# Kernel optimization log

Measured on AMD Instinct MI355X. Metric: run time of the kernel, lower is better.

Reference implementation:

```python
import jax, jax.numpy as jnp
import numpy as np

EPS = float(np.finfo(float).eps)
NUM_RFS = 1

def conv3d(x, w):
    # x: [N,C,D,H,W], w: [O,I,kd,kh,kw], VALID, stride 1 (matches F.conv3d defaults)
    return jax.lax.conv_general_dilated(
        x, w, window_strides=(1, 1, 1), padding='VALID',
        dimension_numbers=('NCDHW', 'OIDHW', 'NCDHW'))

def setup_inputs() -> dict:
    key = jax.random.key(0)
    k1, k2, k3, k4 = jax.random.split(key, 4)
    x = jax.random.normal(k1, (1, 1, 3, 394, 394), jnp.float32)
    x_prev = jax.random.normal(k2, (1, 1, 3, 394, 394), jnp.float32)
    # params stored post-permute as [out_ch, in_ch, kt, kh, kw]
    filts_temp = jax.random.normal(k3, (16, 1, 3, 11, 11), jnp.float32)
    filts_notemp = jax.random.normal(k4, (16, 1, 1, 11, 11), jnp.float32)
    return {"x": x, "x_prev": x_prev, "filts_temp": filts_temp, "filts_notemp": filts_notemp}

def reference(x, x_prev, filts_temp, filts_notemp):
    corr_x = NUM_RFS * filts_temp.shape[3]  # kh
    corr_y = NUM_RFS * filts_temp.shape[4]  # kw
    num_filts = filts_temp.shape[0] + filts_notemp.shape[0]

    def feats(v):
        vt = jax.nn.relu(conv3d(v, filts_temp)) / 2           # [1,16,1,H',W'] (T==kt)
        vn = jax.nn.relu(conv3d(v[:, :, -1:, :, :], filts_notemp))  # last frame, [1,16,1,H',W']
        return jnp.concatenate([vt, vn], axis=1)              # [1,32,1,H',W']

    f = feats(x)
    fp = feats(x_prev)
    # channel-wise normalization
    x1 = f / (jnp.sum(f, axis=1, keepdims=True) + EPS)
    x1_prev = fp / (jnp.sum(fp, axis=1, keepdims=True) + EPS)

    y_max, x_max = x1.shape[3], x1.shape[4]
    yc = y_max - 2 * corr_y
    xc = x_max - 2 * corr_x
    # cropped current-frame channels become conv filters: [nf,1,1,yc,xc]
    x1_filts = x1[:, :, :, corr_y:y_max - corr_y, corr_x:x_max - corr_x].reshape(
        num_filts, 1, 1, yc, xc)
    prev = x1_prev.reshape(1, 1, num_filts, y_max, x_max)
    # normalized cross-correlation via conv3d: out [1, nf, nf, 2cy+1, 2cx+1]
    x2 = conv3d(prev, x1_filts)
    x2 = x2.reshape(1, num_filts, num_filts, 2 * corr_y + 1, 2 * corr_x + 1)
    x2 = x2 / ((y_max - 2 * corr_y) * (x_max - 2 * corr_y))  # faithful to original (uses corr_y twice)
    return x1, x2
```

## Files before the change

### kernel.cpp

```cpp
#include <hip/hip_runtime.h>
#include <hip/hip_bf16.h>


typedef unsigned short ushort_t;
typedef unsigned int uint_t;
typedef unsigned char uchar_t;
typedef __attribute__((ext_vector_type(4))) float f32x4;
typedef __attribute__((ext_vector_type(16))) float f32x16;
typedef __attribute__((ext_vector_type(4))) uint_t uint4_t;
typedef __attribute__((ext_vector_type(2))) uint_t uint2_t;
typedef __attribute__((ext_vector_type(8))) int int8v;

#define EPSF 2.2204460492503131e-16f
#define X1_N (32*384*384)
#define X2_N (32*32*23*23)

#define FILTB_ROW_B 12288
#define FILTB_BYTES (372*48*32*8)
#define PREVB_STRIDE 432
#define PREVB_BYTES (32*385*PREVB_STRIDE)
#define ZERO_BYTES ((size_t)FILTB_BYTES + PREVB_BYTES)
#define FT2_ELEMS (16*45*12)

#define YMAX 367
#define NCHUNKS 16
#define INV_AREA (1.0f/131044.0f)

#define SB_COPY_B 432
#define SB_DYB_B  (8*SB_COPY_B)
#define SB_ROW_B  (4*SB_DYB_B)
#define SB_BYTES  (2*2*SB_ROW_B)

#define SA_BYTES  (8*FILTB_ROW_B)
#define SMEM_TOTAL (SA_BYTES + SB_BYTES)

__device__ __forceinline__ uint_t f32_to_e4m3(float f) {
  if (f < 0.015625f)
    return (uint_t)__float2int_rn(f * 512.0f);
  uint_t b = __builtin_bit_cast(uint_t, f);
  int e = (int)(b >> 23) - 127;
  uint_t m = b & 0x7FFFFFu;
  uint_t keep = m >> 20;
  uint_t rest = m & 0xFFFFFu;
  keep += (rest > 0x80000u) || (rest == 0x80000u && (keep & 1u));
  if (keep == 8u) { keep = 0u; e += 1; }
  if (e > 8) return 0x7Eu;
  return (uint_t)(((e + 7) << 3) | keep);
}

__global__ void prep_kernel(const float* __restrict__ ft, const float* __restrict__ fn,
                            float* __restrict__ fT2)
{
  const int e = blockIdx.x * 256 + threadIdx.x;
  if (e < FT2_ELEMS) {
    const int chp = e / 540;
    const int rem = e - chp * 540;
    const int row = rem / 12;
    const int j = rem - row * 12;
    float v = 0.f;
    if (j < 11) {
      if (row < 33)      v = ft[chp * 363 + row * 11 + j];
      else if (row < 44) v = fn[chp * 121 + (row - 33) * 11 + j];
    }
    fT2[e] = v;
  }
}

__global__ __launch_bounds__(128, 4) void feat_kernel(
    const float* __restrict__ xcur, const float* __restrict__ xprev,
    const float* __restrict__ fT2,
    float* __restrict__ out_x1, uchar_t* __restrict__ prevb)
{
  __shared__ float sPx[3 * 18 * 28];
  __shared__ float sOut[32][9][20];
  const int tid = threadIdx.x;
  const int chp = tid & 15;
  const int r = tid >> 4;
  const int j0 = blockIdx.x * 16;
  const int i0 = blockIdx.y * 8;
  const int i = i0 + r;
  const int mode = blockIdx.z;
  const float* __restrict__ xin = mode ? xprev : xcur;

  for (int e = tid; e < 3 * 18 * 26; e += 128) {
    const int t = e / 468;
    const int rem = e - t * 468;
    const int ri = rem / 26;
    const int ci = rem - ri * 26;
    sPx[(t * 18 + ri) * 28 + ci] = xin[((size_t)t * 394 + i0 + ri) * 394 + j0 + ci];
  }
  __syncthreads();

  const float* __restrict__ fbase = fT2 + chp * 540;

  float accT[16], accN[16];
#pragma unroll
  for (int p = 0; p < 16; ++p) { accT[p] = 0.f; accN[p] = 0.f; }

#pragma unroll
  for (int t = 0; t < 3; ++t) {
    for (int a = 0; a < 11; ++a) {
      const float* row = &sPx[(t * 18 + r + a) * 28];
      float wv[26];
#pragma unroll
      for (int k = 0; k < 6; ++k) {
        const f32x4 q = *(const f32x4*)(row + 4 * k);
        wv[4 * k + 0] = q[0]; wv[4 * k + 1] = q[1];
        wv[4 * k + 2] = q[2]; wv[4 * k + 3] = q[3];
      }
      wv[24] = row[24]; wv[25] = row[25];

      const float* fr = fbase + (t * 11 + a) * 12;
      const f32x4 fq0 = *(const f32x4*)(fr);
      const f32x4 fq1 = *(const f32x4*)(fr + 4);
      const f32x4 fq2 = *(const f32x4*)(fr + 8);
      float fv[12];
#pragma unroll
      for (int k = 0; k < 4; ++k) { fv[k] = fq0[k]; fv[4+k] = fq1[k]; fv[8+k] = fq2[k]; }
      float fv2[12];
      if (t == 2) {
        const float* fr2 = fbase + (33 + a) * 12;
        const f32x4 g0 = *(const f32x4*)(fr2);
        const f32x4 g1 = *(const f32x4*)(fr2 + 4);
        const f32x4 g2 = *(const f32x4*)(fr2 + 8);
#pragma unroll
        for (int k = 0; k < 4; ++k) { fv2[k] = g0[k]; fv2[4+k] = g1[k]; fv2[8+k] = g2[k]; }
      }

#pragma unroll
      for (int b = 0; b < 11; ++b) {
        const float fT = fv[b];
#pragma unroll
        for (int p = 0; p < 16; ++p) accT[p] = fmaf(wv[b + p], fT, accT[p]);
        if (t == 2) {
          const float fN = fv2[b];
#pragma unroll
          for (int p = 0; p < 16; ++p) accN[p] = fmaf(wv[b + p], fN, accN[p]);
        }
      }
    }
  }

  float o0[16], o1[16];
#pragma unroll
  for (int p = 0; p < 16; ++p) {
    const float vT = fmaxf(accT[p], 0.f) * 0.5f;
    const float vN = fmaxf(accN[p], 0.f);
    float s = vT + vN;
    s += __shfl_xor(s, 1);  s += __shfl_xor(s, 2);
    s += __shfl_xor(s, 4);  s += __shfl_xor(s, 8);
    const float inv = 1.f / (s + EPSF);
    o0[p] = vT * inv;
    o1[p] = vN * inv;
  }

  if (mode == 0) {
#pragma unroll
    for (int p = 0; p < 16; ++p) {
      sOut[chp][r][p] = o0[p];
      sOut[chp + 16][r][p] = o1[p];
    }
    __syncthreads();
#pragma unroll
    for (int it = 0; it < 8; ++it) {
      const int idx = it * 128 + tid;
      const int seg = idx & 3;
      const int rr = (idx >> 2) & 7;
      const int chn = idx >> 5;
      const f32x4 v = {sOut[chn][rr][4 * seg], sOut[chn][rr][4 * seg + 1],
                       sOut[chn][rr][4 * seg + 2], sOut[chn][rr][4 * seg + 3]};
      *(f32x4*)(out_x1 + (size_t)chn * 147456 + (i0 + rr) * 384 + j0 + 4 * seg) = v;
    }
  } else {
    uint4_t u0, u1;
#pragma unroll
    for (int q = 0; q < 4; ++q) {
      u0[q] = f32_to_e4m3(o0[4*q]) | (f32_to_e4m3(o0[4*q+1]) << 8) |
              (f32_to_e4m3(o0[4*q+2]) << 16) | (f32_to_e4m3(o0[4*q+3]) << 24);
      u1[q] = f32_to_e4m3(o1[4*q]) | (f32_to_e4m3(o1[4*q+1]) << 8) |
              (f32_to_e4m3(o1[4*q+2]) << 16) | (f32_to_e4m3(o1[4*q+3]) << 24);
    }
    *(uint4_t*)(prevb + ((size_t)chp * 385 + i) * PREVB_STRIDE + j0) = u0;
    *(uint4_t*)(prevb + ((size_t)(chp + 16) * 385 + i) * PREVB_STRIDE + j0) = u1;
  }
}

__global__ __launch_bounds__(256) void pack_kernel(
    const float* __restrict__ x1, uchar_t* __restrict__ filtb)
{
  const int e = blockIdx.x * 256 + threadIdx.x;
  if (e >= 362 * 46 * 32) return;
  const int o = e & 31;
  const int q = e >> 5;
  const int xb = q % 46;
  const int rowr = q / 46 + 5;
  const int i = rowr + 6;
  const int j0 = 11 + xb * 8;
  const float* src = x1 + (size_t)o * 147456 + i * 384 + j0;
  uint_t w0 = 0, w1 = 0;
#pragma unroll
  for (int k = 0; k < 4; ++k) {
    w0 |= f32_to_e4m3((j0 + k     <= 372) ? src[k]     : 0.f) << (8 * k);
    w1 |= f32_to_e4m3((j0 + 4 + k <= 372) ? src[4 + k] : 0.f) << (8 * k);
  }
  uint2_t u = {w0, w1};
  const int off = (xb >> 3) * 2048 + ((xb >> 1) & 1) * 1024 +
                  ((xb >> 2) & 1) * 512 + o * 16 + (xb & 1) * 8;
  *(uint2_t*)(filtb + (size_t)rowr * FILTB_ROW_B + off) = u;
}

__global__ __launch_bounds__(768, 3) void corr_kernel(
    const uchar_t* __restrict__ filtb, const uchar_t* __restrict__ prevb,
    float* __restrict__ x2)
{
  extern __shared__ uchar_t smem[];

  const int tid = threadIdx.x;
  const int lane = tid & 63;
  const int wv = tid >> 6;
  const int cg = (wv >= 6) ? 1 : 0;
  const int gw = wv - 6 * cg;
  const int p = gw >> 1;
  const int kh = gw & 1;
  const int kg = lane >> 5;
  const int nn = lane & 31;

  const int chpair = blockIdx.x / NCHUNKS;
  const int chunk = blockIdx.x % NCHUNKS;
  const int ch = 2 * chpair + cg;
  const int y0 = (chunk * YMAX) / NCHUNKS;
  const int y1 = ((chunk + 1) * YMAX) / NCHUNKS;

  uint_t* const sBg = (uint_t*)(smem + SA_BYTES) + cg * (2 * (SB_ROW_B / 4));

  int boffB[3];
#pragma unroll
  for (int nt = 0; nt < 3; ++nt) {
    const int n = nt * 32 + nn;
    const int dyb = n / 24;
    const int dxr = n - 24 * dyb;
    const int dx = (dxr < 23) ? dxr : 22;
    const int s = dx & 7;
    boffB[nt] = dyb * SB_DYB_B + s * SB_COPY_B + (dx >> 3) * 8 + kg * 32
              + kh * 192;
  }

  const int tl = tid - cg * 384;
  const bool st_act = (tl < 104);
  const int sdyb = st_act ? (tl / 26) : 0;
  const int sg = tl - 26 * (st_act ? (tl / 26) : 0);
  const uchar_t* srcbase = prevb + ((size_t)(ch * 385 + 6 * sdyb)) * PREVB_STRIDE;
  const int dstoff = sdyb * (SB_DYB_B / 4) + 4 * sg;

  uint_t st0 = 0, st1 = 0, st2 = 0, st3 = 0, st4 = 0, st5 = 0;

  auto load_st = [&](int yy) {
    const uint_t* sw = (const uint_t*)(srcbase + (size_t)yy * PREVB_STRIDE) + 4 * sg;
    const uint4_t lo = *(const uint4_t*)(sw);
    const uint2_t hi = *(const uint2_t*)(sw + 4);
    st0 = lo.x; st1 = lo.y; st2 = lo.z; st3 = lo.w; st4 = hi.x; st5 = hi.y;
  };

  auto write_shift = [&](int buf) {
    uint_t* dst = sBg + buf * (SB_ROW_B / 4) + dstoff;
    const uint_t wd[6] = {st0, st1, st2, st3, st4, st5};
#pragma unroll
    for (int s = 0; s < 8; ++s) {
      const int off = s >> 2;
      const int b = (s & 3) * 8;
      uint4_t v;
      if (b == 0) {
        v = uint4_t{wd[off], wd[off + 1], wd[off + 2], wd[off + 3]};
      } else {
        v = uint4_t{(wd[off]     >> b) | (wd[off + 1] << (32 - b)),
                    (wd[off + 1] >> b) | (wd[off + 2] << (32 - b)),
                    (wd[off + 2] >> b) | (wd[off + 3] << (32 - b)),
                    (wd[off + 3] >> b) | (wd[off + 4] << (32 - b))};
      }
      *(uint4_t*)(dst + s * (SB_COPY_B / 4)) = v;
    }
  };

  f32x16 acc[2][3];
#pragma unroll
  for (int m = 0; m < 2; ++m)
#pragma unroll
    for (int nt = 0; nt < 3; ++nt)
#pragma unroll
      for (int r = 0; r < 16; ++r) acc[m][nt][r] = 0.f;

  {
    uint4_t pv[6];
#pragma unroll
    for (int r6 = 0; r6 < 6; ++r6)
      pv[r6] = *(const uint4_t*)(filtb + (size_t)(y0 + r6) * FILTB_ROW_B + tid * 16);
#pragma unroll
    for (int r6 = 0; r6 < 6; ++r6)
      *(uint4_t*)(smem + ((y0 + r6) & 7) * FILTB_ROW_B + tid * 16) = pv[r6];
  }
  if (st_act) {
    load_st(y0);
    write_shift(0);
    if (y0 + 1 < y1) load_st(y0 + 1);
  }

  __syncthreads();

  for (int y = y0; y < y1; ++y) {
    const int pb = (y - y0) & 1;

    const bool a_act = (y + 6 <= y1 + 4);
    uint4_t aval;
    if (a_act)
      aval = *(const uint4_t*)(filtb + (size_t)(y + 6) * FILTB_ROW_B + tid * 16);

    if (st_act && y + 1 < y1) write_shift(pb ^ 1);
    if (st_act && y + 2 < y1) load_st(y + 2);

    const char* sBrd = (const char*)sBg + pb * SB_ROW_B;
    const char* aRow0 = (const char*)smem +
        ((y + 5 - 2 * p) & 7) * FILTB_ROW_B + kh * 6144 + kg * 512 + nn * 16;
    const char* aRow1 = (const char*)smem +
        ((y + 4 - 2 * p) & 7) * FILTB_ROW_B + kh * 6144 + kg * 512 + nn * 16;

#pragma unroll 1
    for (int kt = 0; kt < 3; ++kt) {
      const uint4_t a00 = *(const uint4_t*)(aRow0 + (kt << 11));
      const uint4_t a01 = *(const uint4_t*)(aRow0 + (kt << 11) + 1024);
      const int8v Af0 = {(int)a00.x, (int)a00.y, (int)a00.z, (int)a00.w,
                         (int)a01.x, (int)a01.y, (int)a01.z, (int)a01.w};
      const uint4_t a10 = *(const uint4_t*)(aRow1 + (kt << 11));
      const uint4_t a11 = *(const uint4_t*)(aRow1 + (kt << 11) + 1024);
      const int8v Af1 = {(int)a10.x, (int)a10.y, (int)a10.z, (int)a10.w,
                         (int)a11.x, (int)a11.y, (int)a11.z, (int)a11.w};
#pragma unroll
      for (int nt = 0; nt < 3; ++nt) {
        const char* bp = sBrd + boffB[nt] + (kt << 6);
        const uint2_t b0 = *(const uint2_t*)(bp);
        const uint2_t b1 = *(const uint2_t*)(bp + 8);
        const uint2_t b2 = *(const uint2_t*)(bp + 16);
        const uint2_t b3 = *(const uint2_t*)(bp + 24);
        const int8v Bf = {(int)b0.x, (int)b0.y, (int)b1.x, (int)b1.y,
                          (int)b2.x, (int)b2.y, (int)b3.x, (int)b3.y};
        acc[0][nt] = __builtin_amdgcn_mfma_scale_f32_32x32x64_f8f6f4(
            Af0, Bf, acc[0][nt], 0, 0, 0, 0x7F7F7F7F, 0, 0x7F7F7F7F);
        acc[1][nt] = __builtin_amdgcn_mfma_scale_f32_32x32x64_f8f6f4(
            Af1, Bf, acc[1][nt], 0, 0, 0, 0x7F7F7F7F, 0, 0x7F7F7F7F);
      }
    }

    if (a_act)
      *(uint4_t*)(smem + ((y + 6) & 7) * FILTB_ROW_B + tid * 16) = aval;

    __syncthreads();
  }

#pragma unroll
  for (int m = 0; m < 2; ++m) {
    const int dya = 2 * p + m;
#pragma unroll
    for (int nt = 0; nt < 3; ++nt) {
      const int n = nt * 32 + nn;
      const int dyb = n / 24;
      const int dxr = n - 24 * dyb;
      if (dxr < 23) {
        const int dy = dya + 6 * dyb;
        if (dy <= 22) {
#pragma unroll
          for (int r = 0; r < 16; ++r) {
            const int o = (r & 3) + 8 * (r >> 2) + 4 * kg;
            atomicAdd(&x2[((o * 32 + ch) * 23 + dy) * 23 + dxr],
                      acc[m][nt][r] * INV_AREA);
          }
        }
      }
    }
  }
}

extern "C" void kernel_launch(void* const* d_in, const int* in_sizes, int n_in,
                              void* d_out, int out_size, void* d_ws, size_t ws_size,
                              hipStream_t stream)
{
  const float* x     = (const float*)d_in[0];
  const float* xprev = (const float*)d_in[1];
  const float* ft    = (const float*)d_in[2];
  const float* fn    = (const float*)d_in[3];
  float* out = (float*)d_out;

  uchar_t* filtb = (uchar_t*)d_ws;
  uchar_t* prevb = filtb + FILTB_BYTES;
  float* fT2 = (float*)(prevb + PREVB_BYTES);

  static bool attr_set = false;
  if (!attr_set) {
    (void)hipFuncSetAttribute((const void*)corr_kernel,
        hipFuncAttributeMaxDynamicSharedMemorySize, SMEM_TOTAL);
    attr_set = true;
  }

  hipMemsetAsync(d_ws, 0, ZERO_BYTES, stream);
  hipMemsetAsync(out + X1_N, 0, (size_t)X2_N * sizeof(float), stream);

  prep_kernel<<<dim3((FT2_ELEMS + 255) / 256), 256, 0, stream>>>(ft, fn, fT2);
  feat_kernel<<<dim3(24, 48, 2), 128, 0, stream>>>(x, xprev, fT2, out, prevb);
  pack_kernel<<<dim3((362 * 46 * 32 + 255) / 256), 256, 0, stream>>>(out, filtb);
  corr_kernel<<<dim3(16 * NCHUNKS), 768, SMEM_TOTAL, stream>>>(
      filtb, prevb, out + X1_N);
}
```

Before: 323.1 us.

## Spread B staging across all threads and reduce kh halves in LDS before atomics

```diff
diff --git a/kernel.cpp b/kernel.cpp
--- a/kernel.cpp
+++ b/kernel.cpp
@@ -231,7 +231,8 @@
   const int y0 = (chunk * YMAX) / NCHUNKS;
   const int y1 = ((chunk + 1) * YMAX) / NCHUNKS;
 
-  uint_t* const sBg = (uint_t*)(smem + SA_BYTES) + cg * (2 * (SB_ROW_B / 4));
+  uint_t* const sBall = (uint_t*)(smem + SA_BYTES);
+  uint_t* const sBg = sBall + cg * (2 * (SB_ROW_B / 4));
 
   int boffB[3];
 #pragma unroll
@@ -245,25 +246,23 @@
               + kh * 192;
   }
 
-  const int tl = tid - cg * 384;
-  const bool st_act = (tl < 104);
-  const int sdyb = st_act ? (tl / 26) : 0;
-  const int sg = tl - 26 * (st_act ? (tl / 26) : 0);
-  const uchar_t* srcbase = prevb + ((size_t)(ch * 385 + 6 * sdyb)) * PREVB_STRIDE;
-  const int dstoff = sdyb * (SB_DYB_B / 4) + 4 * sg;
-
-  uint_t st0 = 0, st1 = 0, st2 = 0, st3 = 0, st4 = 0, st5 = 0;
-
-  auto load_st = [&](int yy) {
+  const int btask = tid / 3;
+  const bool b_act = ((tid % 3) == 0) && (btask < 208);
+  const int bgroup = b_act ? (btask / 104) : 0;
+  const int t104 = btask - 104 * (b_act ? (btask / 104) : 0);
+  const int sdyb = b_act ? (t104 / 26) : 0;
+  const int sg = t104 - 26 * (b_act ? (t104 / 26) : 0);
+  const uchar_t* srcbase =
+      prevb + ((size_t)((2 * chpair + bgroup) * 385 + 6 * sdyb)) * PREVB_STRIDE;
+  uint_t* const bdst0 = sBall + bgroup * (2 * (SB_ROW_B / 4)) +
+                        sdyb * (SB_DYB_B / 4) + 4 * sg;
+
+  auto stage_B = [&](int yy, int buf) {
     const uint_t* sw = (const uint_t*)(srcbase + (size_t)yy * PREVB_STRIDE) + 4 * sg;
     const uint4_t lo = *(const uint4_t*)(sw);
     const uint2_t hi = *(const uint2_t*)(sw + 4);
-    st0 = lo.x; st1 = lo.y; st2 = lo.z; st3 = lo.w; st4 = hi.x; st5 = hi.y;
-  };
-
-  auto write_shift = [&](int buf) {
-    uint_t* dst = sBg + buf * (SB_ROW_B / 4) + dstoff;
-    const uint_t wd[6] = {st0, st1, st2, st3, st4, st5};
+    const uint_t wd[6] = {lo.x, lo.y, lo.z, lo.w, hi.x, hi.y};
+    uint_t* dst = bdst0 + buf * (SB_ROW_B / 4);
 #pragma unroll
     for (int s = 0; s < 8; ++s) {
       const int off = s >> 2;
@@ -289,21 +288,13 @@
 #pragma unroll
       for (int r = 0; r < 16; ++r) acc[m][nt][r] = 0.f;
 
-  {
-    uint4_t pv[6];
-#pragma unroll
-    for (int r6 = 0; r6 < 6; ++r6)
-      pv[r6] = *(const uint4_t*)(filtb + (size_t)(y0 + r6) * FILTB_ROW_B + tid * 16);
-#pragma unroll
-    for (int r6 = 0; r6 < 6; ++r6)
-      *(uint4_t*)(smem + ((y0 + r6) & 7) * FILTB_ROW_B + tid * 16) = pv[r6];
-  }
-  if (st_act) {
-    load_st(y0);
-    write_shift(0);
-    if (y0 + 1 < y1) load_st(y0 + 1);
-  }
-
+#pragma unroll 1
+  for (int r6 = 0; r6 < 6; ++r6) {
+    const uint4_t v = *(const uint4_t*)(
+        filtb + (size_t)(y0 + r6) * FILTB_ROW_B + tid * 16);
+    *(uint4_t*)(smem + ((y0 + r6) & 7) * FILTB_ROW_B + tid * 16) = v;
+  }
+  if (b_act) stage_B(y0, 0);
   __syncthreads();
 
   for (int y = y0; y < y1; ++y) {
@@ -314,23 +305,21 @@
     if (a_act)
       aval = *(const uint4_t*)(filtb + (size_t)(y + 6) * FILTB_ROW_B + tid * 16);
 
-    if (st_act && y + 1 < y1) write_shift(pb ^ 1);
-    if (st_act && y + 2 < y1) load_st(y + 2);
-
     const char* sBrd = (const char*)sBg + pb * SB_ROW_B;
     const char* aRow0 = (const char*)smem +
-        ((y + 5 - 2 * p) & 7) * FILTB_ROW_B + kh * 6144 + kg * 512 + nn * 16;
+        ((y + 5 - 2 * p) & 7) * FILTB_ROW_B + kg * 512 + nn * 16;
     const char* aRow1 = (const char*)smem +
-        ((y + 4 - 2 * p) & 7) * FILTB_ROW_B + kh * 6144 + kg * 512 + nn * 16;
+        ((y + 4 - 2 * p) & 7) * FILTB_ROW_B + kg * 512 + nn * 16;
 
 #pragma unroll 1
     for (int kt = 0; kt < 3; ++kt) {
-      const uint4_t a00 = *(const uint4_t*)(aRow0 + (kt << 11));
-      const uint4_t a01 = *(const uint4_t*)(aRow0 + (kt << 11) + 1024);
+      const int ktg = kh * 3 + kt;
+      const uint4_t a00 = *(const uint4_t*)(aRow0 + (ktg << 11));
+      const uint4_t a01 = *(const uint4_t*)(aRow0 + (ktg << 11) + 1024);
       const int8v Af0 = {(int)a00.x, (int)a00.y, (int)a00.z, (int)a00.w,
                          (int)a01.x, (int)a01.y, (int)a01.z, (int)a01.w};
-      const uint4_t a10 = *(const uint4_t*)(aRow1 + (kt << 11));
-      const uint4_t a11 = *(const uint4_t*)(aRow1 + (kt << 11) + 1024);
+      const uint4_t a10 = *(const uint4_t*)(aRow1 + (ktg << 11));
+      const uint4_t a11 = *(const uint4_t*)(aRow1 + (ktg << 11) + 1024);
       const int8v Af1 = {(int)a10.x, (int)a10.y, (int)a10.z, (int)a10.w,
                          (int)a11.x, (int)a11.y, (int)a11.z, (int)a11.w};
 #pragma unroll
@@ -351,26 +340,62 @@
 
     if (a_act)
       *(uint4_t*)(smem + ((y + 6) & 7) * FILTB_ROW_B + tid * 16) = aval;
+    if (b_act && y + 1 < y1) stage_B(y + 1, pb ^ 1);
 
     __syncthreads();
   }
 
-#pragma unroll
-  for (int m = 0; m < 2; ++m) {
-    const int dya = 2 * p + m;
-#pragma unroll
-    for (int nt = 0; nt < 3; ++nt) {
-      const int n = nt * 32 + nn;
-      const int dyb = n / 24;
-      const int dxr = n - 24 * dyb;
-      if (dxr < 23) {
-        const int dy = dya + 6 * dyb;
-        if (dy <= 22) {
-#pragma unroll
-          for (int r = 0; r < 16; ++r) {
-            const int o = (r & 3) + 8 * (r >> 2) + 4 * kg;
-            atomicAdd(&x2[((o * 32 + ch) * 23 + dy) * 23 + dxr],
-                      acc[m][nt][r] * INV_AREA);
+  {
+    uchar_t* const rbase =
+        smem + ((size_t)(cg * 3 + p) * 24 * 64 + lane) * 16;
+    if (kh == 1) {
+      int q = 0;
+#pragma unroll
+      for (int m = 0; m < 2; ++m)
+#pragma unroll
+        for (int nt = 0; nt < 3; ++nt)
+#pragma unroll
+          for (int seg = 0; seg < 4; ++seg) {
+            const f32x4 v = {acc[m][nt][4 * seg], acc[m][nt][4 * seg + 1],
+                             acc[m][nt][4 * seg + 2], acc[m][nt][4 * seg + 3]};
+            *(f32x4*)(rbase + q * 1024) = v;
+            ++q;
+          }
+    }
+    __syncthreads();
+    if (kh == 0) {
+      int q = 0;
+#pragma unroll
+      for (int m = 0; m < 2; ++m)
+#pragma unroll
+        for (int nt = 0; nt < 3; ++nt)
+#pragma unroll
+          for (int seg = 0; seg < 4; ++seg) {
+            const f32x4 v = *(const f32x4*)(rbase + q * 1024);
+            acc[m][nt][4 * seg] += v[0];
+            acc[m][nt][4 * seg + 1] += v[1];
+            acc[m][nt][4 * seg + 2] += v[2];
+            acc[m][nt][4 * seg + 3] += v[3];
+            ++q;
+          }
+#pragma unroll
+      for (int m = 0; m < 2; ++m) {
+        const int dya = 2 * p + m;
+#pragma unroll
+        for (int nt = 0; nt < 3; ++nt) {
+          const int n = nt * 32 + nn;
+          const int dyb = n / 24;
+          const int dxr = n - 24 * dyb;
+          if (dxr < 23) {
+            const int dy = dya + 6 * dyb;
+            if (dy <= 22) {
+#pragma unroll
+              for (int r = 0; r < 16; ++r) {
+                const int o = (r & 3) + 8 * (r >> 2) + 4 * kg;
+                atomicAdd(&x2[((o * 32 + ch) * 23 + dy) * 23 + dxr],
+                          acc[m][nt][r] * INV_AREA);
+              }
+            }
           }
         }
       }
```

Measured after the change: 275.0 us. 14.9% less time.
